# Kernel tuning notes

Measured on AMD Instinct MI355X. Metric: run time of the kernel, lower is better.

Reference implementation:

```python
import jax, jax.numpy as jnp
import numpy as np

N, E = 20000, 640000
F_IN, H, T = 64, 256, 64  # in_channels = T, edge_attr dim = T -> EdgeConv MLP in = 3*T


def _lin(key, fan_in, fan_out):
    k1, k2 = jax.random.split(key)
    s = 1.0 / np.sqrt(fan_in)
    W = jax.random.uniform(k1, (fan_in, fan_out), jnp.float32, -s, s)
    b = jax.random.uniform(k2, (fan_out,), jnp.float32, -s, s)
    return W, b


def setup_inputs() -> dict:
    key = jax.random.key(0)
    ks = jax.random.split(key, 12)
    x = jax.random.normal(ks[0], (N, F_IN), jnp.float32)
    edge_index = jax.random.randint(ks[1], (2, E), 0, N, jnp.int32)
    edge_attr = jax.random.normal(ks[2], (E, T), jnp.float32)
    conv1_W, conv1_b = _lin(ks[3], F_IN, H)
    e_W1, e_b1 = _lin(ks[4], 3 * T, H)
    e_W2, e_b2 = _lin(ks[5], H, H)
    conv2_W, conv2_b = _lin(ks[6], 2 * H, H)
    conv3_W, conv3_b = _lin(ks[7], H, F_IN)
    lin1_W, lin1_b = _lin(ks[8], 2 * F_IN, F_IN)
    lin2_W, lin2_b = _lin(ks[9], F_IN, 128)
    lin3_W, lin3_b = _lin(ks[10], 128, 32)
    lin4_W, lin4_b = _lin(ks[11], 32, 2)
    return dict(x=x, edge_index=edge_index, edge_attr=edge_attr,
                conv1_W=conv1_W, conv1_b=conv1_b,
                e_W1=e_W1, e_b1=e_b1, e_W2=e_W2, e_b2=e_b2,
                conv2_W=conv2_W, conv2_b=conv2_b,
                conv3_W=conv3_W, conv3_b=conv3_b,
                lin1_W=lin1_W, lin1_b=lin1_b, lin2_W=lin2_W, lin2_b=lin2_b,
                lin3_W=lin3_W, lin3_b=lin3_b, lin4_W=lin4_W, lin4_b=lin4_b)


def reference(x, edge_index, edge_attr,
              conv1_W, conv1_b, e_W1, e_b1, e_W2, e_b2,
              conv2_W, conv2_b, conv3_W, conv3_b,
              lin1_W, lin1_b, lin2_W, lin2_b, lin3_W, lin3_b, lin4_W, lin4_b):
    n = x.shape[0]
    src, dst = edge_index[0], edge_index[1]
    # GCN symmetric norm with self-loops (deg counted on dst, +1 for self-loop)
    deg = jax.ops.segment_sum(jnp.ones_like(src, jnp.float32), dst, num_segments=n) + 1.0
    dis = jax.lax.rsqrt(deg)

    def gcn(h, W, b):
        hw = h @ W
        msg = hw[src] * (dis[src] * dis[dst])[:, None]
        # self-loop contribution: norm = dis[i]^2
        return jax.ops.segment_sum(msg, dst, num_segments=n) + hw * (dis * dis)[:, None] + b

    out1 = jax.nn.relu(gcn(x, conv1_W, conv1_b))
    # EdgeConv: MLP(cat[x_i, x_j, edge_attr]) with max aggregation onto dst (x_i = target)
    m = jnp.concatenate([x[dst], x[src], edge_attr], axis=1)      # [E, 3T]
    m = jax.nn.relu(m @ e_W1 + e_b1) @ e_W2 + e_b2                 # [E, H]
    agg = jax.ops.segment_max(m, dst, num_segments=n)
    agg = jnp.where(jnp.isfinite(agg), agg, 0.0)                   # nodes with no in-edges
    out_e1 = jax.nn.relu(agg)

    out2 = jax.nn.relu(gcn(jnp.concatenate([out1, out_e1], axis=1), conv2_W, conv2_b))
    out3 = jax.nn.relu(gcn(out2, conv3_W, conv3_b))
    h = jnp.concatenate([x, out3], axis=1)
    h = jax.nn.softplus(h @ lin1_W + lin1_b)
    h = jax.nn.softplus(h @ lin2_W + lin2_b)
    h = jax.nn.softplus(h @ lin3_W + lin3_b)
    h = h @ lin4_W + lin4_b                                        # [N, 2]
    return (h[:, 0], h[:, 1])
```

## Files before the change

### kernel.cpp

```cpp
#include <hip/hip_runtime.h>
#include <stdint.h>

typedef __bf16 bf16x8 __attribute__((ext_vector_type(8)));
typedef float f32x4 __attribute__((ext_vector_type(4)));
typedef unsigned long long ull_t;

#define DEV __device__ __forceinline__

DEV unsigned short f2bf(float f) {
  unsigned int u = __float_as_uint(f);
  return (unsigned short)((u + 0x7FFFu + ((u >> 16) & 1u)) >> 16);
}

DEV float bf2f(unsigned short b) { return __uint_as_float((unsigned int)b << 16); }

DEV f32x4 zero4() { f32x4 z = {0.f, 0.f, 0.f, 0.f}; return z; }

DEV float softplusf(float v) { return (v > 15.f) ? v : log1pf(expf(v)); }

__global__ void pack_weight(const float* __restrict__ W, unsigned short* __restrict__ P,
                            int K, int Ncols) {
  int idx = blockIdx.x * 256 + threadIdx.x;
  if (idx >= K * Ncols) return;
  int j = idx & 7;
  int lane = (idx >> 3) & 63;
  int rest = idx >> 9;
  int NT = Ncols >> 4;
  int nt = rest % NT;
  int kt = rest / NT;
  int k = kt * 32 + ((j >> 2) * 16) + ((lane >> 4) * 4) + (j & 3);
  int col = nt * 16 + (lane & 15);
  P[idx] = f2bf(W[(size_t)k * Ncols + col]);
}

__global__ void k_deg(const int* __restrict__ dst, int* __restrict__ degi, int E) {
  int i = blockIdx.x * 256 + threadIdx.x;
  if (i < E) atomicAdd(&degi[dst[i]], 1);
}

__global__ void k_dis(const int* __restrict__ degi, float* __restrict__ dis, int n) {
  int i = blockIdx.x * 256 + threadIdx.x;
  if (i < n) dis[i] = rsqrtf((float)degi[i] + 1.0f);
}

__global__ __launch_bounds__(1024) void k_scan(const int* __restrict__ degi,
                                               int* __restrict__ ptr, int n) {
  __shared__ int part[1024];
  const int tid = threadIdx.x;
  const int chunk = (n + 1023) / 1024;
  const int b = tid * chunk;
  const int e2 = min(n, b + chunk);
  int s = 0;
  for (int i = b; i < e2; ++i) s += degi[i];
  part[tid] = s;
  __syncthreads();
  for (int off = 1; off < 1024; off <<= 1) {
    int val = (tid >= off) ? part[tid - off] : 0;
    __syncthreads();
    part[tid] += val;
    __syncthreads();
  }
  int run = (tid == 0) ? 0 : part[tid - 1];
  for (int i = b; i < e2; ++i) {
    ptr[i] = run;
    run += degi[i];
  }
  if (tid == 1023) ptr[n] = run;
}

__global__ void k_fill(const int* __restrict__ srcs, const int* __restrict__ dsts,
                       const int* __restrict__ ptr, const float* __restrict__ dis,
                       int* __restrict__ fillc,
                       int2* __restrict__ sc_s, int* __restrict__ dst_s,
                       int* __restrict__ perm_s, int E) {
  int e = blockIdx.x * 256 + threadIdx.x;
  if (e >= E) return;
  int d = dsts[e];
  int s = srcs[e];
  int pos = ptr[d] + atomicAdd(&fillc[d], 1);
  float c = dis[s] * dis[d];
  sc_s[pos] = make_int2(s, __float_as_int(c));
  dst_s[pos] = d;
  perm_s[pos] = e;
}

template <int COLS, bool FINALIZE>
__global__ __launch_bounds__(256) void k_gather_agg(
    const float* __restrict__ feat, const int2* __restrict__ sc,
    const int* __restrict__ ptr, const float* __restrict__ dis,
    const float* __restrict__ hw, const float* __restrict__ bias,
    float* __restrict__ out, int n) {
  constexpr int V = COLS / 64;
  const int v = blockIdx.x * 4 + (threadIdx.x >> 6);
  if (v >= n) return;
  const int lane = threadIdx.x & 63;
  const int beg = ptr[v], end = ptr[v + 1];
  float acc[V];
#pragma unroll
  for (int i = 0; i < V; ++i) acc[i] = 0.f;
  const int cnt = end - beg;
  const int2* scp = sc + beg;
  int i = 0;
  for (; i + 4 <= cnt; i += 4) {
    int2 s0 = scp[i], s1 = scp[i + 1], s2 = scp[i + 2], s3 = scp[i + 3];
    float c0 = __int_as_float(s0.y), c1 = __int_as_float(s1.y);
    float c2 = __int_as_float(s2.y), c3 = __int_as_float(s3.y);
    const float* r0 = feat + (size_t)s0.x * COLS + lane * V;
    const float* r1 = feat + (size_t)s1.x * COLS + lane * V;
    const float* r2 = feat + (size_t)s2.x * COLS + lane * V;
    const float* r3 = feat + (size_t)s3.x * COLS + lane * V;
    if constexpr (V == 4) {
      float4 f0 = *(const float4*)r0, f1 = *(const float4*)r1;
      float4 f2 = *(const float4*)r2, f3 = *(const float4*)r3;
      acc[0] += f0.x * c0 + f1.x * c1 + f2.x * c2 + f3.x * c3;
      acc[1] += f0.y * c0 + f1.y * c1 + f2.y * c2 + f3.y * c3;
      acc[2] += f0.z * c0 + f1.z * c1 + f2.z * c2 + f3.z * c3;
      acc[3] += f0.w * c0 + f1.w * c1 + f2.w * c2 + f3.w * c3;
    } else {
      acc[0] += r0[0] * c0 + r1[0] * c1 + r2[0] * c2 + r3[0] * c3;
    }
  }
  for (; i < cnt; ++i) {
    int2 s0 = scp[i];
    float c0 = __int_as_float(s0.y);
    const float* r0 = feat + (size_t)s0.x * COLS + lane * V;
    if constexpr (V == 4) {
      float4 f0 = *(const float4*)r0;
      acc[0] += f0.x * c0; acc[1] += f0.y * c0; acc[2] += f0.z * c0; acc[3] += f0.w * c0;
    } else {
      acc[0] += r0[0] * c0;
    }
  }
  float* op = out + (size_t)v * COLS + lane * V;
  if constexpr (FINALIZE) {
    const float dv = dis[v];
    float d2 = dv * dv;
    const float* hp = hw + (size_t)v * COLS + lane * V;
#pragma unroll
    for (int i2 = 0; i2 < V; ++i2)
      acc[i2] = fmaxf(acc[i2] + hp[i2] * d2 + bias[lane * V + i2], 0.f);
  }
  if constexpr (V == 4) {
    *(float4*)op = make_float4(acc[0], acc[1], acc[2], acc[3]);
  } else {
    op[0] = acc[0];
  }
}

template <int K, int NOUT, bool COMPOSE, bool RELUBIAS>
__global__ __launch_bounds__(256, 2) void gcn_gemm(
    const float* __restrict__ inA, const float* __restrict__ inB,
    const float* __restrict__ dis,
    const unsigned short* __restrict__ Wp, const float* __restrict__ bias,
    float* __restrict__ out, int out_stride, int nrows) {
  constexpr int NT = NOUT / 16;
  constexpr int NTW = NOUT / 64;
  __shared__ unsigned short s_in[64 * K];
  const int tid = threadIdx.x;
  const int r0 = blockIdx.x * 64;

  constexpr int C4R = K / 4;
  for (int idx = tid; idx < 64 * C4R; idx += 256) {
    int row = idx / C4R;
    int rem = idx - row * C4R;
    int grow = r0 + row;
    float4 v = make_float4(0.f, 0.f, 0.f, 0.f);
    if (grow < nrows) {
      v = *(const float4*)&inA[(size_t)grow * K + rem * 4];
      if constexpr (COMPOSE) {
        float d = dis[grow];
        d *= d;
        float4 w2 = *(const float4*)&inB[(size_t)grow * K + rem * 4];
        v.x += w2.x * d; v.y += w2.y * d; v.z += w2.z * d; v.w += w2.w * d;
      }
    }
    ushort4 b;
    b.x = f2bf(v.x); b.y = f2bf(v.y); b.z = f2bf(v.z); b.w = f2bf(v.w);
    *(ushort4*)&s_in[row * K + ((rem ^ (row & 7)) * 4)] = b;
  }
  __syncthreads();

  const int lane = tid & 63, wid = tid >> 6;
  const int lr = lane & 15, lg = lane >> 4;
  f32x4 acc[4][NTW];
#pragma unroll
  for (int m = 0; m < 4; ++m)
#pragma unroll
    for (int n2 = 0; n2 < NTW; ++n2) acc[m][n2] = zero4();

#pragma unroll
  for (int kt = 0; kt < K / 32; ++kt) {
    bf16x8 a[4];
#pragma unroll
    for (int m = 0; m < 4; ++m) {
      int rA = m * 16 + lr;
      int c1 = (kt * 8 + lg) ^ (rA & 7);
      int c2 = (kt * 8 + lg + 4) ^ (rA & 7);
      union { bf16x8 v; ull_t q[2]; } u;
      u.q[0] = *(const ull_t*)&s_in[rA * K + c1 * 4];
      u.q[1] = *(const ull_t*)&s_in[rA * K + c2 * 4];
      a[m] = u.v;
    }
#pragma unroll
    for (int n2 = 0; n2 < NTW; ++n2) {
      int nt = wid * NTW + n2;
      bf16x8 b = *(const bf16x8*)&Wp[(((size_t)kt * NT + nt) * 64 + lane) * 8];
#pragma unroll
      for (int m = 0; m < 4; ++m)
        acc[m][n2] = __builtin_amdgcn_mfma_f32_16x16x32_bf16(a[m], b, acc[m][n2], 0, 0, 0);
    }
  }

#pragma unroll
  for (int n2 = 0; n2 < NTW; ++n2) {
    int col = (wid * NTW + n2) * 16 + lr;
    float bv = 0.f;
    if (RELUBIAS) bv = bias[col];
#pragma unroll
    for (int m = 0; m < 4; ++m) {
#pragma unroll
      for (int r = 0; r < 4; ++r) {
        int grow = r0 + m * 16 + lg * 4 + r;
        if (grow < nrows) {
          float v = acc[m][n2][r];
          if (RELUBIAS) v = fmaxf(v + bv, 0.f);
          out[(size_t)grow * out_stride + col] = v;
        }
      }
    }
  }
}

__global__ __launch_bounds__(512, 4) void k_edgeconv(
    const float* __restrict__ x, const float* __restrict__ ea,
    const int2* __restrict__ sc_s, const int* __restrict__ dst_s,
    const int* __restrict__ perm_s,
    const unsigned short* __restrict__ W1p, const float* __restrict__ b1,
    const unsigned short* __restrict__ W2p, const float* __restrict__ b2,
    float* __restrict__ h2, int E) {
  __shared__ unsigned short s_buf[64 * 256];
  __shared__ int s_src[64], s_dst[64], s_perm[64];
  const int tid = threadIdx.x;
  const int e0 = blockIdx.x * 64;
  if (tid < 64) {
    int e = e0 + tid;
    s_src[tid] = (e < E) ? sc_s[e].x : 0;
    s_dst[tid] = (e < E) ? dst_s[e] : 0;
    s_perm[tid] = (e < E) ? perm_s[e] : 0;
  }
  __syncthreads();
#pragma unroll
  for (int seg = 0; seg < 3; ++seg) {
#pragma unroll
    for (int it = 0; it < 2; ++it) {
      int idx = it * 512 + tid;
      int ei = idx >> 4;
      int q = idx & 15;
      const float* row;
      if (seg == 0) row = x + (size_t)s_dst[ei] * 64;
      else if (seg == 1) row = x + (size_t)s_src[ei] * 64;
      else row = ea + (size_t)s_perm[ei] * 64;
      float4 v = make_float4(0.f, 0.f, 0.f, 0.f);
      if (e0 + ei < E) v = *(const float4*)(row + q * 4);
      ushort4 b;
      b.x = f2bf(v.x); b.y = f2bf(v.y); b.z = f2bf(v.z); b.w = f2bf(v.w);
      int chunk = (seg * 16 + q) ^ (ei & 7);
      *(ushort4*)&s_buf[ei * 192 + chunk * 4] = b;
    }
  }
  __syncthreads();

  const int lane = tid & 63, wid = tid >> 6;
  const int wr = wid >> 2;
  const int wc = wid & 3;
  const int lr = lane & 15, lg = lane >> 4;
  f32x4 acc[2][4];
#pragma unroll
  for (int m = 0; m < 2; ++m)
#pragma unroll
    for (int n2 = 0; n2 < 4; ++n2) acc[m][n2] = zero4();

#pragma unroll
  for (int kt = 0; kt < 6; ++kt) {
    bf16x8 a[2];
#pragma unroll
    for (int m = 0; m < 2; ++m) {
      int rA = wr * 32 + m * 16 + lr;
      int rr = rA & 7;
      union { bf16x8 v; ull_t q[2]; } u;
      u.q[0] = *(const ull_t*)&s_buf[rA * 192 + ((kt * 8 + lg) ^ rr) * 4];
      u.q[1] = *(const ull_t*)&s_buf[rA * 192 + ((kt * 8 + lg + 4) ^ rr) * 4];
      a[m] = u.v;
    }
#pragma unroll
    for (int n2 = 0; n2 < 4; ++n2) {
      int nt = wc * 4 + n2;
      bf16x8 b = *(const bf16x8*)&W1p[(((size_t)kt * 16 + nt) * 64 + lane) * 8];
#pragma unroll
      for (int m = 0; m < 2; ++m)
        acc[m][n2] = __builtin_amdgcn_mfma_f32_16x16x32_bf16(a[m], b, acc[m][n2], 0, 0, 0);
    }
  }
  __syncthreads();

#pragma unroll
  for (int n2 = 0; n2 < 4; ++n2) {
    int col = (wc * 4 + n2) * 16 + lr;
    float bv = b1[col];
    int chunk0 = col >> 2, cm = col & 3;
#pragma unroll
    for (int m = 0; m < 2; ++m)
#pragma unroll
      for (int r = 0; r < 4; ++r) {
        int row = wr * 32 + m * 16 + lg * 4 + r;
        float v = fmaxf(acc[m][n2][r] + bv, 0.f);
        s_buf[row * 256 + ((chunk0 ^ (row & 7)) * 4) + cm] = f2bf(v);
      }
  }
  __syncthreads();

#pragma unroll
  for (int m = 0; m < 2; ++m)
#pragma unroll
    for (int n2 = 0; n2 < 4; ++n2) acc[m][n2] = zero4();
#pragma unroll
  for (int kt = 0; kt < 8; ++kt) {
    bf16x8 a[2];
#pragma unroll
    for (int m = 0; m < 2; ++m) {
      int rA = wr * 32 + m * 16 + lr;
      int rr = rA & 7;
      union { bf16x8 v; ull_t q[2]; } u;
      u.q[0] = *(const ull_t*)&s_buf[rA * 256 + ((kt * 8 + lg) ^ rr) * 4];
      u.q[1] = *(const ull_t*)&s_buf[rA * 256 + ((kt * 8 + lg + 4) ^ rr) * 4];
      a[m] = u.v;
    }
#pragma unroll
    for (int n2 = 0; n2 < 4; ++n2) {
      int nt = wc * 4 + n2;
      bf16x8 b = *(const bf16x8*)&W2p[(((size_t)kt * 16 + nt) * 64 + lane) * 8];
#pragma unroll
      for (int m = 0; m < 2; ++m)
        acc[m][n2] = __builtin_amdgcn_mfma_f32_16x16x32_bf16(a[m], b, acc[m][n2], 0, 0, 0);
    }
  }
  __syncthreads();

#pragma unroll
  for (int n2 = 0; n2 < 4; ++n2) {
    int col = (wc * 4 + n2) * 16 + lr;
    float bv = b2[col];
    int chunk0 = col >> 2, cm = col & 3;
#pragma unroll
    for (int m = 0; m < 2; ++m)
#pragma unroll
      for (int r = 0; r < 4; ++r) {
        int row = wr * 32 + m * 16 + lg * 4 + r;
        float v = (e0 + row < E) ? fmaxf(acc[m][n2][r] + bv, 0.f) : 0.f;
        s_buf[row * 256 + ((chunk0 ^ (row & 7)) * 4) + cm] = f2bf(v);
      }
  }
  __syncthreads();

  {
    const int col = tid & 255;
    const int half = tid >> 8;
    const int rbeg = half * 32;
    const int chunk0 = col >> 2, cm = col & 3;
    float run = 0.f;
    int cur = s_dst[rbeg];
    for (int r = rbeg; r < rbeg + 32; ++r) {
      int d2 = s_dst[r];
      if (d2 != cur) {
        if (run > 0.f)
          atomicMax((int*)&h2[(size_t)cur * 512 + 256 + col], __float_as_int(run));
        run = 0.f;
        cur = d2;
      }
      run = fmaxf(run, bf2f(s_buf[r * 256 + ((chunk0 ^ (r & 7)) * 4) + cm]));
    }
    if (run > 0.f)
      atomicMax((int*)&h2[(size_t)cur * 512 + 256 + col], __float_as_int(run));
  }
}

__global__ __launch_bounds__(256) void k_head(
    const float* __restrict__ x, const float* __restrict__ out3,
    const float* __restrict__ W1, const float* __restrict__ b1,
    const float* __restrict__ W2, const float* __restrict__ b2,
    const float* __restrict__ W3, const float* __restrict__ b3,
    const float* __restrict__ W4, const float* __restrict__ b4,
    float* __restrict__ out, int n) {
  __shared__ float sW1[128 * 64];
  __shared__ float sW3[128 * 32];
  __shared__ float sW4[32 * 2];
  __shared__ float sb1[64], sb2[128], sb3[32], sb4[2];
  __shared__ float sbuf[4][352];
  const int tid = threadIdx.x;
  for (int i = tid; i < 128 * 64; i += 256) sW1[i] = W1[i];
  for (int i = tid; i < 128 * 32; i += 256) sW3[i] = W3[i];
  if (tid < 64) sW4[tid] = W4[tid];
  if (tid < 64) sb1[tid] = b1[tid];
  if (tid < 128) sb2[tid] = b2[tid];
  if (tid < 32) sb3[tid] = b3[tid];
  if (tid < 2) sb4[tid] = b4[tid];
  __syncthreads();
  const int wid = tid >> 6, lane = tid & 63;
  float* B = sbuf[wid];
  const int per = gridDim.x * 4;
  const int iters = (n + per - 1) / per;
  for (int it = 0; it < iters; ++it) {
    const int node = it * per + blockIdx.x * 4 + wid;
    const bool act = node < n;
    if (act) {
      B[lane] = x[(size_t)node * 64 + lane];
      B[64 + lane] = out3[(size_t)node * 64 + lane];
    }
    __syncthreads();
    if (act) {
      float o = sb1[lane];
#pragma unroll 8
      for (int k = 0; k < 128; ++k) o += B[k] * sW1[k * 64 + lane];
      B[128 + lane] = softplusf(o);
    }
    __syncthreads();
    if (act) {
      float o0 = sb2[lane], o1 = sb2[64 + lane];
#pragma unroll 8
      for (int k = 0; k < 64; ++k) {
        float v = B[128 + k];
        o0 += v * W2[k * 128 + lane];
        o1 += v * W2[k * 128 + 64 + lane];
      }
      B[192 + lane] = softplusf(o0);
      B[256 + lane] = softplusf(o1);
    }
    __syncthreads();
    if (act && lane < 32) {
      float o = sb3[lane];
#pragma unroll 8
      for (int k = 0; k < 128; ++k) o += B[192 + k] * sW3[k * 32 + lane];
      B[320 + lane] = softplusf(o);
    }
    __syncthreads();
    if (act && lane < 2) {
      float o = sb4[lane];
#pragma unroll
      for (int k = 0; k < 32; ++k) o += B[320 + k] * sW4[k * 2 + lane];
      out[(size_t)lane * n + node] = o;
    }
    __syncthreads();
  }
}

static inline size_t alignup(size_t v) { return (v + 255) & ~(size_t)255; }

extern "C" void kernel_launch(void* const* d_in, const int* in_sizes, int n_in,
                              void* d_out, int out_size, void* d_ws, size_t ws_size,
                              hipStream_t stream) {
  const float* x = (const float*)d_in[0];
  const int* ei = (const int*)d_in[1];
  const float* ea = (const float*)d_in[2];
  const float* c1W = (const float*)d_in[3];
  const float* c1b = (const float*)d_in[4];
  const float* eW1 = (const float*)d_in[5];
  const float* eb1 = (const float*)d_in[6];
  const float* eW2 = (const float*)d_in[7];
  const float* eb2 = (const float*)d_in[8];
  const float* c2W = (const float*)d_in[9];
  const float* c2b = (const float*)d_in[10];
  const float* c3W = (const float*)d_in[11];
  const float* c3b = (const float*)d_in[12];
  const float* l1W = (const float*)d_in[13];
  const float* l1b = (const float*)d_in[14];
  const float* l2W = (const float*)d_in[15];
  const float* l2b = (const float*)d_in[16];
  const float* l3W = (const float*)d_in[17];
  const float* l3b = (const float*)d_in[18];
  const float* l4W = (const float*)d_in[19];
  const float* l4b = (const float*)d_in[20];
  const int n = in_sizes[0] / 64;
  const int E = in_sizes[1] / 2;
  const int* srcs = ei;
  const int* dsts = ei + E;

  char* w = (char*)d_ws;
  auto alloc = [&](size_t bytes) {
    char* p = w;
    w += alignup(bytes);
    return p;
  };
  float* dis = (float*)alloc((size_t)n * 4);
  int* degi = (int*)alloc((size_t)n * 4);
  int* ptr = (int*)alloc((size_t)(n + 1) * 4);
  int* fillc = (int*)alloc((size_t)n * 4);
  int2* sc_s = (int2*)alloc((size_t)E * 8);
  int* dst_s = (int*)alloc((size_t)E * 4);
  int* perm_s = (int*)alloc((size_t)E * 4);
  float* agg1 = (float*)alloc((size_t)n * 64 * 4);
  float* h2 = (float*)alloc((size_t)n * 512 * 4);
  float* hw2 = (float*)alloc((size_t)n * 256 * 4);
  float* out2 = (float*)alloc((size_t)n * 256 * 4);
  float* hw3 = (float*)alloc((size_t)n * 64 * 4);
  float* out3 = (float*)alloc((size_t)n * 64 * 4);
  unsigned short* p_c1 = (unsigned short*)alloc(64 * 256 * 2);
  unsigned short* p_e1 = (unsigned short*)alloc(192 * 256 * 2);
  unsigned short* p_e2 = (unsigned short*)alloc(256 * 256 * 2);
  unsigned short* p_c2 = (unsigned short*)alloc(512 * 256 * 2);
  unsigned short* p_c3 = (unsigned short*)alloc(256 * 64 * 2);

  hipMemsetAsync(degi, 0, (size_t)n * 4, stream);
  hipMemsetAsync(fillc, 0, (size_t)n * 4, stream);
  hipMemsetAsync(h2, 0, (size_t)n * 512 * 4, stream);

  pack_weight<<<(64 * 256) / 256, 256, 0, stream>>>(c1W, p_c1, 64, 256);
  pack_weight<<<(192 * 256) / 256, 256, 0, stream>>>(eW1, p_e1, 192, 256);
  pack_weight<<<(256 * 256) / 256, 256, 0, stream>>>(eW2, p_e2, 256, 256);
  pack_weight<<<(512 * 256) / 256, 256, 0, stream>>>(c2W, p_c2, 512, 256);
  pack_weight<<<(256 * 64) / 256, 256, 0, stream>>>(c3W, p_c3, 256, 64);

  k_deg<<<(E + 255) / 256, 256, 0, stream>>>(dsts, degi, E);
  k_dis<<<(n + 255) / 256, 256, 0, stream>>>(degi, dis, n);
  k_scan<<<1, 1024, 0, stream>>>(degi, ptr, n);
  k_fill<<<(E + 255) / 256, 256, 0, stream>>>(srcs, dsts, ptr, dis, fillc,
                                              sc_s, dst_s, perm_s, E);

  const int ablocks = (n + 3) / 4;
  const int gblocks = (n + 63) / 64;

  k_gather_agg<64, false><<<ablocks, 256, 0, stream>>>(x, sc_s, ptr, dis,
                                                       nullptr, nullptr, agg1, n);
  gcn_gemm<64, 256, true, true><<<gblocks, 256, 0, stream>>>(agg1, x, dis, p_c1, c1b, h2, 512, n);

  k_edgeconv<<<(E + 63) / 64, 512, 0, stream>>>(x, ea, sc_s, dst_s, perm_s,
                                                p_e1, eb1, p_e2, eb2, h2, E);

  gcn_gemm<512, 256, false, false><<<gblocks, 256, 0, stream>>>(h2, nullptr, nullptr, p_c2, nullptr, hw2, 256, n);
  k_gather_agg<256, true><<<ablocks, 256, 0, stream>>>(hw2, sc_s, ptr, dis,
                                                       hw2, c2b, out2, n);

  gcn_gemm<256, 64, false, false><<<gblocks, 256, 0, stream>>>(out2, nullptr, nullptr, p_c3, nullptr, hw3, 64, n);
  k_gather_agg<64, true><<<ablocks, 256, 0, stream>>>(hw3, sc_s, ptr, dis,
                                                      hw3, c3b, out3, n);

  k_head<<<320, 256, 0, stream>>>(x, out3, l1W, l1b, l2W, l2b, l3W, l3b, l4W, l4b,
                                  (float*)d_out, n);
}
```

Measured before the change: 693.7 us.

## Store GCN projected features in bf16 and transpose edgeconv max-reduction buffer

The conv2 and conv3 GEMMs now write their projected features (hw2, hw3) as bf16, and the gather-aggregate kernels read and widen them. This halves the bytes moved in the random-access neighbor gathers. Separately, the edgeconv epilogue stores results column-major with padding, so the segment-max pass can read 8 rows per vector load instead of scalar swizzled reads. The head kernel grid grows from 320 to 1250 blocks. The bf16 intermediates add rounding error to the GCN aggregations.

```diff
diff --git a/kernel.cpp b/kernel.cpp
--- a/kernel.cpp
+++ b/kernel.cpp
@@ -3,7 +3,9 @@
 
 typedef __bf16 bf16x8 __attribute__((ext_vector_type(8)));
 typedef float f32x4 __attribute__((ext_vector_type(4)));
+typedef unsigned short u16x8 __attribute__((ext_vector_type(8)));
 typedef unsigned long long ull_t;
+typedef unsigned short ushort_t;
 
 #define DEV __device__ __forceinline__
 
@@ -84,17 +86,38 @@
   perm_s[pos] = e;
 }
 
-template <int COLS, bool FINALIZE>
+template <int COLS, bool FINALIZE, bool INBF16>
 __global__ __launch_bounds__(256) void k_gather_agg(
-    const float* __restrict__ feat, const int2* __restrict__ sc,
+    const void* __restrict__ featv, const int2* __restrict__ sc,
     const int* __restrict__ ptr, const float* __restrict__ dis,
-    const float* __restrict__ hw, const float* __restrict__ bias,
+    const void* __restrict__ hwv, const float* __restrict__ bias,
     float* __restrict__ out, int n) {
   constexpr int V = COLS / 64;
   const int v = blockIdx.x * 4 + (threadIdx.x >> 6);
   if (v >= n) return;
   const int lane = threadIdx.x & 63;
   const int beg = ptr[v], end = ptr[v + 1];
+
+  auto loadrow = [&](int s, float* f) {
+    if constexpr (INBF16) {
+      const ushort_t* feat = (const ushort_t*)featv;
+      if constexpr (V == 4) {
+        ushort4 u = *(const ushort4*)(feat + (size_t)s * COLS + lane * 4);
+        f[0] = bf2f(u.x); f[1] = bf2f(u.y); f[2] = bf2f(u.z); f[3] = bf2f(u.w);
+      } else {
+        f[0] = bf2f(feat[(size_t)s * COLS + lane]);
+      }
+    } else {
+      const float* feat = (const float*)featv;
+      if constexpr (V == 4) {
+        float4 q = *(const float4*)(feat + (size_t)s * COLS + lane * 4);
+        f[0] = q.x; f[1] = q.y; f[2] = q.z; f[3] = q.w;
+      } else {
+        f[0] = feat[(size_t)s * COLS + lane];
+      }
+    }
+  };
+
   float acc[V];
 #pragma unroll
   for (int i = 0; i < V; ++i) acc[i] = 0.f;
@@ -103,42 +126,47 @@
   int i = 0;
   for (; i + 4 <= cnt; i += 4) {
     int2 s0 = scp[i], s1 = scp[i + 1], s2 = scp[i + 2], s3 = scp[i + 3];
+    float f0[V], f1[V], f2[V], f3[V];
+    loadrow(s0.x, f0); loadrow(s1.x, f1); loadrow(s2.x, f2); loadrow(s3.x, f3);
     float c0 = __int_as_float(s0.y), c1 = __int_as_float(s1.y);
     float c2 = __int_as_float(s2.y), c3 = __int_as_float(s3.y);
-    const float* r0 = feat + (size_t)s0.x * COLS + lane * V;
-    const float* r1 = feat + (size_t)s1.x * COLS + lane * V;
-    const float* r2 = feat + (size_t)s2.x * COLS + lane * V;
-    const float* r3 = feat + (size_t)s3.x * COLS + lane * V;
-    if constexpr (V == 4) {
-      float4 f0 = *(const float4*)r0, f1 = *(const float4*)r1;
-      float4 f2 = *(const float4*)r2, f3 = *(const float4*)r3;
-      acc[0] += f0.x * c0 + f1.x * c1 + f2.x * c2 + f3.x * c3;
-      acc[1] += f0.y * c0 + f1.y * c1 + f2.y * c2 + f3.y * c3;
-      acc[2] += f0.z * c0 + f1.z * c1 + f2.z * c2 + f3.z * c3;
-      acc[3] += f0.w * c0 + f1.w * c1 + f2.w * c2 + f3.w * c3;
-    } else {
-      acc[0] += r0[0] * c0 + r1[0] * c1 + r2[0] * c2 + r3[0] * c3;
-    }
+#pragma unroll
+    for (int j = 0; j < V; ++j)
+      acc[j] += f0[j] * c0 + f1[j] * c1 + f2[j] * c2 + f3[j] * c3;
   }
   for (; i < cnt; ++i) {
     int2 s0 = scp[i];
     float c0 = __int_as_float(s0.y);
-    const float* r0 = feat + (size_t)s0.x * COLS + lane * V;
-    if constexpr (V == 4) {
-      float4 f0 = *(const float4*)r0;
-      acc[0] += f0.x * c0; acc[1] += f0.y * c0; acc[2] += f0.z * c0; acc[3] += f0.w * c0;
-    } else {
-      acc[0] += r0[0] * c0;
-    }
+    float f0[V];
+    loadrow(s0.x, f0);
+#pragma unroll
+    for (int j = 0; j < V; ++j) acc[j] += f0[j] * c0;
   }
   float* op = out + (size_t)v * COLS + lane * V;
   if constexpr (FINALIZE) {
     const float dv = dis[v];
     float d2 = dv * dv;
-    const float* hp = hw + (size_t)v * COLS + lane * V;
+    float h[V];
+    if constexpr (INBF16) {
+      const ushort_t* hw = (const ushort_t*)hwv;
+      if constexpr (V == 4) {
+        ushort4 u = *(const ushort4*)(hw + (size_t)v * COLS + lane * 4);
+        h[0] = bf2f(u.x); h[1] = bf2f(u.y); h[2] = bf2f(u.z); h[3] = bf2f(u.w);
+      } else {
+        h[0] = bf2f(hw[(size_t)v * COLS + lane]);
+      }
+    } else {
+      const float* hw = (const float*)hwv;
+      if constexpr (V == 4) {
+        float4 q = *(const float4*)(hw + (size_t)v * COLS + lane * 4);
+        h[0] = q.x; h[1] = q.y; h[2] = q.z; h[3] = q.w;
+      } else {
+        h[0] = hw[(size_t)v * COLS + lane];
+      }
+    }
 #pragma unroll
     for (int i2 = 0; i2 < V; ++i2)
-      acc[i2] = fmaxf(acc[i2] + hp[i2] * d2 + bias[lane * V + i2], 0.f);
+      acc[i2] = fmaxf(acc[i2] + h[i2] * d2 + bias[lane * V + i2], 0.f);
   }
   if constexpr (V == 4) {
     *(float4*)op = make_float4(acc[0], acc[1], acc[2], acc[3]);
@@ -147,12 +175,12 @@
   }
 }
 
-template <int K, int NOUT, bool COMPOSE, bool RELUBIAS>
+template <int K, int NOUT, bool COMPOSE, bool RELUBIAS, bool OUTBF16>
 __global__ __launch_bounds__(256, 2) void gcn_gemm(
     const float* __restrict__ inA, const float* __restrict__ inB,
     const float* __restrict__ dis,
     const unsigned short* __restrict__ Wp, const float* __restrict__ bias,
-    float* __restrict__ out, int out_stride, int nrows) {
+    void* __restrict__ outv, int out_stride, int nrows) {
   constexpr int NT = NOUT / 16;
   constexpr int NTW = NOUT / 64;
   __shared__ unsigned short s_in[64 * K];
@@ -224,7 +252,11 @@
         if (grow < nrows) {
           float v = acc[m][n2][r];
           if (RELUBIAS) v = fmaxf(v + bv, 0.f);
-          out[(size_t)grow * out_stride + col] = v;
+          if constexpr (OUTBF16) {
+            ((ushort_t*)outv)[(size_t)grow * out_stride + col] = f2bf(v);
+          } else {
+            ((float*)outv)[(size_t)grow * out_stride + col] = v;
+          }
         }
       }
     }
@@ -238,7 +270,7 @@
     const unsigned short* __restrict__ W1p, const float* __restrict__ b1,
     const unsigned short* __restrict__ W2p, const float* __restrict__ b2,
     float* __restrict__ h2, int E) {
-  __shared__ unsigned short s_buf[64 * 256];
+  __shared__ unsigned short s_buf[256 * 72];
   __shared__ int s_src[64], s_dst[64], s_perm[64];
   const int tid = threadIdx.x;
   const int e0 = blockIdx.x * 64;
@@ -350,15 +382,18 @@
   for (int n2 = 0; n2 < 4; ++n2) {
     int col = (wc * 4 + n2) * 16 + lr;
     float bv = b2[col];
-    int chunk0 = col >> 2, cm = col & 3;
-#pragma unroll
-    for (int m = 0; m < 2; ++m)
+#pragma unroll
+    for (int m = 0; m < 2; ++m) {
+      int rbase = wr * 32 + m * 16 + lg * 4;
+      ull_t pk = 0;
 #pragma unroll
       for (int r = 0; r < 4; ++r) {
-        int row = wr * 32 + m * 16 + lg * 4 + r;
+        int row = rbase + r;
         float v = (e0 + row < E) ? fmaxf(acc[m][n2][r] + bv, 0.f) : 0.f;
-        s_buf[row * 256 + ((chunk0 ^ (row & 7)) * 4) + cm] = f2bf(v);
-      }
+        pk |= ((ull_t)f2bf(v)) << (16 * r);
+      }
+      *(ull_t*)&s_buf[col * 72 + rbase] = pk;
+    }
   }
   __syncthreads();
 
@@ -366,18 +401,23 @@
     const int col = tid & 255;
     const int half = tid >> 8;
     const int rbeg = half * 32;
-    const int chunk0 = col >> 2, cm = col & 3;
     float run = 0.f;
     int cur = s_dst[rbeg];
-    for (int r = rbeg; r < rbeg + 32; ++r) {
-      int d2 = s_dst[r];
-      if (d2 != cur) {
-        if (run > 0.f)
-          atomicMax((int*)&h2[(size_t)cur * 512 + 256 + col], __float_as_int(run));
-        run = 0.f;
-        cur = d2;
-      }
-      run = fmaxf(run, bf2f(s_buf[r * 256 + ((chunk0 ^ (r & 7)) * 4) + cm]));
+#pragma unroll
+    for (int i = 0; i < 4; ++i) {
+      u16x8 pack = *(const u16x8*)&s_buf[col * 72 + rbeg + i * 8];
+#pragma unroll
+      for (int r2 = 0; r2 < 8; ++r2) {
+        int r = rbeg + i * 8 + r2;
+        int d2 = s_dst[r];
+        if (d2 != cur) {
+          if (run > 0.f)
+            atomicMax((int*)&h2[(size_t)cur * 512 + 256 + col], __float_as_int(run));
+          run = 0.f;
+          cur = d2;
+        }
+        run = fmaxf(run, bf2f(pack[r2]));
+      }
     }
     if (run > 0.f)
       atomicMax((int*)&h2[(size_t)cur * 512 + 256 + col], __float_as_int(run));
@@ -499,9 +539,9 @@
   int* perm_s = (int*)alloc((size_t)E * 4);
   float* agg1 = (float*)alloc((size_t)n * 64 * 4);
   float* h2 = (float*)alloc((size_t)n * 512 * 4);
-  float* hw2 = (float*)alloc((size_t)n * 256 * 4);
+  ushort_t* hw2b = (ushort_t*)alloc((size_t)n * 256 * 2);
   float* out2 = (float*)alloc((size_t)n * 256 * 4);
-  float* hw3 = (float*)alloc((size_t)n * 64 * 4);
+  ushort_t* hw3b = (ushort_t*)alloc((size_t)n * 64 * 2);
   float* out3 = (float*)alloc((size_t)n * 64 * 4);
   unsigned short* p_c1 = (unsigned short*)alloc(64 * 256 * 2);
   unsigned short* p_e1 = (unsigned short*)alloc(192 * 256 * 2);
@@ -528,21 +568,24 @@
   const int ablocks = (n + 3) / 4;
   const int gblocks = (n + 63) / 64;
 
-  k_gather_agg<64, false><<<ablocks, 256, 0, stream>>>(x, sc_s, ptr, dis,
-                                                       nullptr, nullptr, agg1, n);
-  gcn_gemm<64, 256, true, true><<<gblocks, 256, 0, stream>>>(agg1, x, dis, p_c1, c1b, h2, 512, n);
+  k_gather_agg<64, false, false><<<ablocks, 256, 0, stream>>>(
+      x, sc_s, ptr, dis, nullptr, nullptr, agg1, n);
+  gcn_gemm<64, 256, true, true, false><<<gblocks, 256, 0, stream>>>(
+      agg1, x, dis, p_c1, c1b, h2, 512, n);
 
   k_edgeconv<<<(E + 63) / 64, 512, 0, stream>>>(x, ea, sc_s, dst_s, perm_s,
                                                 p_e1, eb1, p_e2, eb2, h2, E);
 
-  gcn_gemm<512, 256, false, false><<<gblocks, 256, 0, stream>>>(h2, nullptr, nullptr, p_c2, nullptr, hw2, 256, n);
-  k_gather_agg<256, true><<<ablocks, 256, 0, stream>>>(hw2, sc_s, ptr, dis,
-                                                       hw2, c2b, out2, n);
-
-  gcn_gemm<256, 64, false, false><<<gblocks, 256, 0, stream>>>(out2, nullptr, nullptr, p_c3, nullptr, hw3, 64, n);
-  k_gather_agg<64, true><<<ablocks, 256, 0, stream>>>(hw3, sc_s, ptr, dis,
-                                                      hw3, c3b, out3, n);
-
-  k_head<<<320, 256, 0, stream>>>(x, out3, l1W, l1b, l2W, l2b, l3W, l3b, l4W, l4b,
-                                  (float*)d_out, n);
-}
+  gcn_gemm<512, 256, false, false, true><<<gblocks, 256, 0, stream>>>(
+      h2, nullptr, nullptr, p_c2, nullptr, hw2b, 256, n);
+  k_gather_agg<256, true, true><<<ablocks, 256, 0, stream>>>(
+      hw2b, sc_s, ptr, dis, hw2b, c2b, out2, n);
+
+  gcn_gemm<256, 64, false, false, true><<<gblocks, 256, 0, stream>>>(
+      out2, nullptr, nullptr, p_c3, nullptr, hw3b, 64, n);
+  k_gather_agg<64, true, true><<<ablocks, 256, 0, stream>>>(
+      hw3b, sc_s, ptr, dis, hw3b, c3b, out3, n);
+
+  k_head<<<1250, 256, 0, stream>>>(x, out3, l1W, l1b, l2W, l2b, l3W, l3b, l4W, l4b,
+                                   (float*)d_out, n);
+}
```

After: 620.9 us. 10.5% less time.
